# Performance work log

Hardware: AMD Instinct MI355X
Metric: run time of the kernel (lower is better)

## Reference

```python
import jax, jax.numpy as jnp
import numpy as np

B = 4096          # number of sampled constraints (batch)
H = 1024          # hidden_size
N_UNIT = 5
MAXD = 4          # max(DEPTHS)
TAU = 1.0
N_STEPS = N_UNIT * (1 + 2 * MAXD)  # 45
CLIST = np.linspace(10.0, 20.0, 5).astype(np.float32)
NSC = 11
DEPTH_VALS = np.array([2, 3, 4])
RATIO_VALS = np.array([3, 4, 6])
KS_VALS = np.array([3, 5, 7])


def setup_inputs() -> dict:
    key = jax.random.key(0)
    ks = jax.random.split(key, 20)
    def p(k, shape):
        return jax.random.uniform(k, shape, minval=-0.1, maxval=0.1, dtype=jnp.float32)
    return {
        'constraints': jax.random.uniform(ks[0], (B,), minval=10.0, maxval=20.0, dtype=jnp.float32),
        'superclass_id': 3,
        'gumbel_u': jax.random.uniform(ks[1], (N_STEPS, B, 3), minval=1e-6, maxval=1.0 - 1e-6, dtype=jnp.float32),
        'cond_emb': p(ks[2], (len(CLIST), H // 2)),
        'sc_emb': p(ks[3], (NSC, H // 2)),
        'depth_emb': p(ks[4], (3, H)),
        'ratio_emb': p(ks[5], (3, H)),
        'ks_emb': p(ks[6], (3, H)),
        'W_ih': p(ks[7], (4 * H, H)), 'b_ih': p(ks[8], (4 * H,)),
        'W_hh': p(ks[9], (4 * H, H)), 'b_hh': p(ks[10], (4 * H,)),
        'depth_W': p(ks[11], (3, H)), 'depth_b': p(ks[12], (3,)),
        'width_W': p(ks[13], (3, H)), 'width_b': p(ks[14], (3,)),
        'ks_W': p(ks[15], (3, H)), 'ks_b': p(ks[16], (3,)),
    }


def reference(constraints, superclass_id, gumbel_u, cond_emb, sc_emb, depth_emb, ratio_emb,
              ks_emb, W_ih, b_ih, W_hh, b_hh, depth_W, depth_b, width_W, width_b, ks_W, ks_b):
    clist = jnp.asarray(CLIST)
    # linear_interpolation: find bracketing interval for each constraint
    idx = jnp.clip(jnp.searchsorted(clist, constraints, side='right') - 1, 0, clist.shape[0] - 2)
    left, right = clist[idx], clist[idx + 1]
    w = ((right - constraints) / (right - left))[:, None]
    cemb = w * cond_emb[idx] + (1.0 - w) * cond_emb[idx + 1]          # [B, H/2]
    sce = jnp.broadcast_to(sc_emb[superclass_id], (constraints.shape[0], sc_emb.shape[1]))
    embed = jnp.concatenate([cemb, sce], axis=1)                       # [B, H]
    h = jnp.zeros((constraints.shape[0], H), embed.dtype)
    c = h

    def lstm(x, h, c):
        gates = x @ W_ih.T + b_ih + h @ W_hh.T + b_hh                  # [B, 4H]
        i, f, g, o = jnp.split(gates, 4, axis=-1)
        c2 = jax.nn.sigmoid(f) * c + jax.nn.sigmoid(i) * jnp.tanh(g)
        h2 = jax.nn.sigmoid(o) * jnp.tanh(c2)
        return h2, c2

    def gsample(logits, u):
        g = -jnp.log(-jnp.log(u))
        y_soft = jax.nn.softmax((logits + g) / TAU, axis=-1)
        onehot = jax.nn.one_hot(jnp.argmax(y_soft, -1), logits.shape[-1], dtype=y_soft.dtype)
        y_hard = onehot - jax.lax.stop_gradient(y_soft) + y_soft       # straight-through
        return jnp.argmax(y_hard, -1), y_soft, y_hard

    t = 0
    d_idx, d_probs, d_wbs = [], [], []
    r_idx, r_probs, r_wbs = [], [], []
    k_idx, k_probs, k_wbs = [], [], []
    for _unit in range(N_UNIT):
        h, c = lstm(embed, h, c)
        s, ys, yh = gsample(h @ depth_W.T + depth_b, gumbel_u[t]); t += 1
        d_idx.append(s); d_probs.append(ys); d_wbs.append(yh)
        embed = depth_emb[s]
        for _blk in range(MAXD):
            h, c = lstm(embed, h, c)
            s, ys, yh = gsample(h @ width_W.T + width_b, gumbel_u[t]); t += 1
            r_idx.append(s); r_probs.append(ys); r_wbs.append(yh)
            embed = ratio_emb[s]
            h, c = lstm(embed, h, c)
            s, ys, yh = gsample(h @ ks_W.T + ks_b, gumbel_u[t]); t += 1
            k_idx.append(s); k_probs.append(ys); k_wbs.append(yh)
            embed = ks_emb[s]

    depths = jnp.asarray(DEPTH_VALS)[jnp.stack(d_idx)]   # [5, B]
    ratios = jnp.asarray(RATIO_VALS)[jnp.stack(r_idx)]   # [20, B]
    kss = jnp.asarray(KS_VALS)[jnp.stack(k_idx)]         # [20, B]
    return (depths, ratios, kss,
            jnp.stack(d_wbs), jnp.stack(d_probs),
            jnp.stack(r_wbs), jnp.stack(r_probs),
            jnp.stack(k_wbs), jnp.stack(k_probs))
```

## Files before the change

kernel.cpp:

```cpp
#include <hip/hip_runtime.h>
#include <cmath>

namespace {

typedef _Float16 f16;
typedef f16 f16x8 __attribute__((ext_vector_type(8)));
typedef f16 f16x4 __attribute__((ext_vector_type(4)));
typedef float f32x4 __attribute__((ext_vector_type(4)));

constexpr int B  = 4096;
constexpr int H  = 1024;
constexpr int FH = 4 * H;
constexpr int NSTEPS = 45;
constexpr float INVS = 1.0f / 2048.0f;

__device__ __forceinline__ float sigf(float x) { return 1.0f / (1.0f + expf(-x)); }

struct HL { f16 h, l; };
__device__ __forceinline__ HL split16(float a) {
  float ah = (float)(f16)a;
  if (fabsf(a) < 6.1035156e-5f) ah = 0.0f;
  HL r; r.h = (f16)ah; r.l = (f16)((a - ah) * 2048.0f); return r;
}

__device__ __forceinline__ void async16(f16* lds_dst, const f16* gsrc) {
  __builtin_amdgcn_global_load_lds(
      (const __attribute__((address_space(1))) void*)gsrc,
      (__attribute__((address_space(3))) void*)lds_dst, 16, 0, 0);
}

__global__ void convertW_kernel(const float* __restrict__ W,
                                f16* __restrict__ Whi, f16* __restrict__ Wlo) {
  size_t i = ((size_t)blockIdx.x * 256 + threadIdx.x) * 4;
  float4 v = *(const float4*)(W + i);
  HL a = split16(v.x), b = split16(v.y), c = split16(v.z), d = split16(v.w);
  f16x4 hi = {a.h, b.h, c.h, d.h};
  f16x4 lo = {a.l, b.l, c.l, d.l};
  *(f16x4*)(Whi + i) = hi;
  *(f16x4*)(Wlo + i) = lo;
}

__global__ void precompute_kernel(
    const float* __restrict__ W_ih, const float* __restrict__ b_ih, const float* __restrict__ b_hh,
    const float* __restrict__ depth_emb, const float* __restrict__ ratio_emb, const float* __restrict__ ks_emb,
    const float* __restrict__ cond_emb, const float* __restrict__ sc_emb, const int* __restrict__ sid_p,
    float* __restrict__ tblD, float* __restrict__ tblR, float* __restrict__ tblK,
    float* __restrict__ condp, float* __restrict__ base0) {
  const int w4   = threadIdx.x >> 6;
  const int lane = threadIdx.x & 63;
  const int j    = blockIdx.x * 4 + w4;
  const float* wr = W_ih + (size_t)j * H;
  const int k = lane * 16;
  float4 wv0 = *(const float4*)(wr + k);
  float4 wv1 = *(const float4*)(wr + k + 4);
  float4 wv2 = *(const float4*)(wr + k + 8);
  float4 wv3 = *(const float4*)(wr + k + 12);

  auto dot = [&](const float* e) -> float {
    float4 e0 = *(const float4*)(e);
    float4 e1 = *(const float4*)(e + 4);
    float4 e2 = *(const float4*)(e + 8);
    float4 e3 = *(const float4*)(e + 12);
    return e0.x*wv0.x + e0.y*wv0.y + e0.z*wv0.z + e0.w*wv0.w
         + e1.x*wv1.x + e1.y*wv1.y + e1.z*wv1.z + e1.w*wv1.w
         + e2.x*wv2.x + e2.y*wv2.y + e2.z*wv2.z + e2.w*wv2.w
         + e3.x*wv3.x + e3.y*wv3.y + e3.z*wv3.z + e3.w*wv3.w;
  };

  float a[15];
  a[0] = dot(depth_emb + k);       a[1] = dot(depth_emb + H + k);   a[2] = dot(depth_emb + 2*H + k);
  a[3] = dot(ratio_emb + k);       a[4] = dot(ratio_emb + H + k);   a[5] = dot(ratio_emb + 2*H + k);
  a[6] = dot(ks_emb + k);          a[7] = dot(ks_emb + H + k);      a[8] = dot(ks_emb + 2*H + k);
  a[9] = a[10] = a[11] = a[12] = a[13] = a[14] = 0.0f;
  constexpr int HH = H / 2;
  int sid = sid_p[0];
  if (lane < 32) {
    a[9]  = dot(cond_emb + 0*HH + k);
    a[10] = dot(cond_emb + 1*HH + k);
    a[11] = dot(cond_emb + 2*HH + k);
    a[12] = dot(cond_emb + 3*HH + k);
    a[13] = dot(cond_emb + 4*HH + k);
  } else {
    a[14] = dot(sc_emb + sid*HH + (k - HH));
  }
  #pragma unroll
  for (int i = 0; i < 15; ++i) {
    #pragma unroll
    for (int off = 32; off > 0; off >>= 1) a[i] += __shfl_xor(a[i], off);
  }
  if (lane == 0) {
    float bias = b_ih[j] + b_hh[j];
    tblD[0*FH+j]=a[0]+bias; tblD[1*FH+j]=a[1]+bias; tblD[2*FH+j]=a[2]+bias;
    tblR[0*FH+j]=a[3]+bias; tblR[1*FH+j]=a[4]+bias; tblR[2*FH+j]=a[5]+bias;
    tblK[0*FH+j]=a[6]+bias; tblK[1*FH+j]=a[7]+bias; tblK[2*FH+j]=a[8]+bias;
    condp[0*FH+j]=a[9]; condp[1*FH+j]=a[10]; condp[2*FH+j]=a[11];
    condp[3*FH+j]=a[12]; condp[4*FH+j]=a[13];
    base0[j] = a[14] + bias;
  }
}

__global__ void step0_kernel(const float* __restrict__ constraints,
                             const float* __restrict__ condp, const float* __restrict__ base0,
                             f16* __restrict__ hhi, f16* __restrict__ hlo, float* __restrict__ c) {
  int idx = blockIdx.x * blockDim.x + threadIdx.x;
  int b = idx >> 10;
  int j = idx & (H - 1);
  float cv = constraints[b];
  int i0 = 0;
  if (cv >= 12.5f) i0 = 1;
  if (cv >= 15.0f) i0 = 2;
  if (cv >= 17.5f) i0 = 3;
  float right = 10.0f + 2.5f * (float)(i0 + 1);
  float w = (right - cv) / 2.5f;
  const float* c0 = condp + (size_t)i0 * FH;
  const float* c1 = c0 + FH;
  float iw = 1.0f - w;
  float xi = w*c0[j]       + iw*c1[j]       + base0[j];
  float xg = w*c0[2*H+j]   + iw*c1[2*H+j]   + base0[2*H+j];
  float xo = w*c0[3*H+j]   + iw*c1[3*H+j]   + base0[3*H+j];
  float cn = sigf(xi) * tanhf(xg);
  float hn = sigf(xo) * tanhf(cn);
  c[idx] = cn;
  HL s = split16(hn);
  hhi[idx] = s.h; hlo[idx] = s.l;
}

constexpr int BUFE = 24576;

__global__ __launch_bounds__(512, 2) void lstm_step_mfma(
    const f16* __restrict__ hhi, const f16* __restrict__ hlo,
    f16* __restrict__ nhhi, f16* __restrict__ nhlo,
    float* __restrict__ cbuf,
    const f16* __restrict__ Whi, const f16* __restrict__ Wlo,
    const float* __restrict__ tbl, const int* __restrict__ sel) {
  __shared__ __align__(16) f16 lds[3 * BUFE];

  const int tid  = threadIdx.x;
  const int lane = tid & 63;
  const int w    = tid >> 6;
  const int wm   = w >> 1, wn = w & 1;
  const int l15  = lane & 15;
  const int kq   = lane >> 4;

  const int L   = blockIdx.x;
  const int xcd = L & 7, seq = L >> 3;
  const int jb  = (xcd << 2) + (seq & 3);
  const int bb  = seq >> 2;
  const int b0  = bb << 8;
  const int j0  = jb << 5;

  f32x4 accH[4][4] = {};
  f32x4 accL[4][4] = {};

  int offA[4], offB[4];
  #pragma unroll
  for (int mf = 0; mf < 4; ++mf) {
    int R = wm * 64 + mf * 16 + l15;
    int c = kq ^ (R & 3) ^ ((R >> 2) & 3);
    offA[mf] = R * 32 + c * 8;
  }
  #pragma unroll
  for (int nf = 0; nf < 4; ++nf) {
    int R = nf * 32 + wn * 16 + l15;
    int c = kq ^ (R & 3) ^ ((R >> 2) & 3);
    offB[nf] = 16384 + R * 32 + c * 8;
  }

  const int rs = tid >> 2, cs = tid & 3;
  const int r1 = 128 + rs;
  const int cl0 = cs ^ (rs & 3) ^ ((rs >> 2) & 3);
  const int cl1 = cs ^ (r1 & 3) ^ ((r1 >> 2) & 3);
  const int wrow = ((rs >> 5) << 10) + j0 + (rs & 31);
  const f16* sA0h = hhi + (size_t)(b0 + rs) * H + cl0 * 8;
  const f16* sA0l = hlo + (size_t)(b0 + rs) * H + cl0 * 8;
  const f16* sA1h = hhi + (size_t)(b0 + r1) * H + cl1 * 8;
  const f16* sA1l = hlo + (size_t)(b0 + r1) * H + cl1 * 8;
  const f16* sBh  = Whi + (size_t)wrow * H + cl0 * 8;
  const f16* sBl  = Wlo + (size_t)wrow * H + cl0 * 8;
  const int dA0 = w * 512, dA1 = 4096 + w * 512, dB = 16384 + w * 512;

  auto stage6 = [&](f16* buf, int ko) {
    async16(buf + dA0,        sA0h + ko);
    async16(buf + dA0 + 8192, sA0l + ko);
    async16(buf + dA1,        sA1h + ko);
    async16(buf + dA1 + 8192, sA1l + ko);
    async16(buf + dB,         sBh + ko);
    async16(buf + dB + 4096,  sBl + ko);
  };

  f16 *bA = lds, *bB = lds + BUFE, *bC = lds + 2 * BUFE;
  stage6(bA, 0);
  stage6(bB, 32);
  asm volatile("s_waitcnt vmcnt(6)" ::: "memory");
  __builtin_amdgcn_s_barrier();

  for (int kt = 0; kt < 32; ++kt) {
    if (kt < 30) stage6(bC, (kt + 2) * 32);

    f16x8 bh[4], bl[4];
    #pragma unroll
    for (int nf = 0; nf < 4; ++nf) {
      bh[nf] = *(const f16x8*)(bA + offB[nf]);
      bl[nf] = *(const f16x8*)(bA + offB[nf] + 4096);
    }
    #pragma unroll
    for (int mf = 0; mf < 4; ++mf) {
      f16x8 ah = *(const f16x8*)(bA + offA[mf]);
      f16x8 al = *(const f16x8*)(bA + offA[mf] + 8192);
      #pragma unroll
      for (int nf = 0; nf < 4; ++nf) {
        accH[mf][nf] = __builtin_amdgcn_mfma_f32_16x16x32_f16(ah, bh[nf], accH[mf][nf], 0, 0, 0);
        accL[mf][nf] = __builtin_amdgcn_mfma_f32_16x16x32_f16(ah, bl[nf], accL[mf][nf], 0, 0, 0);
        accL[mf][nf] = __builtin_amdgcn_mfma_f32_16x16x32_f16(al, bh[nf], accL[mf][nf], 0, 0, 0);
      }
    }

    if (kt < 30)       asm volatile("s_waitcnt vmcnt(6)" ::: "memory");
    else if (kt == 30) asm volatile("s_waitcnt vmcnt(0)" ::: "memory");
    if (kt < 31) __builtin_amdgcn_s_barrier();

    f16* t = bA; bA = bB; bB = bC; bC = t;
  }

  const int j = j0 + wn * 16 + l15;
  #pragma unroll
  for (int mf = 0; mf < 4; ++mf) {
    #pragma unroll
    for (int r = 0; r < 4; ++r) {
      int b = b0 + wm * 64 + mf * 16 + kq * 4 + r;
      int s = sel[b];
      const float* t = tbl + (size_t)s * FH + j;
      float gi = accH[mf][0][r] + accL[mf][0][r] * INVS + t[0];
      float gf = accH[mf][1][r] + accL[mf][1][r] * INVS + t[H];
      float gg = accH[mf][2][r] + accL[mf][2][r] * INVS + t[2*H];
      float go = accH[mf][3][r] + accL[mf][3][r] * INVS + t[3*H];
      size_t off = (size_t)b * H + j;
      float cp = cbuf[off];
      float cn = sigf(gf) * cp + sigf(gi) * tanhf(gg);
      float hn = sigf(go) * tanhf(cn);
      cbuf[off] = cn;
      HL sp = split16(hn);
      nhhi[off] = sp.h;
      nhlo[off] = sp.l;
    }
  }
}

__global__ void sampler_kernel(const f16* __restrict__ hhi, const f16* __restrict__ hlo,
                               const float* __restrict__ selW, const float* __restrict__ selb,
                               const float* __restrict__ gu,
                               float* __restrict__ val_out, float* __restrict__ wb_out,
                               float* __restrict__ p_out,
                               float v0, float v1, float v2,
                               int* __restrict__ sel) {
  int wave = threadIdx.x >> 6;
  int lane = threadIdx.x & 63;
  int b = blockIdx.x * 4 + wave;
  const f16* hh = hhi + (size_t)b * H;
  const f16* hl = hlo + (size_t)b * H;
  float acc0 = 0, acc1 = 0, acc2 = 0;
  #pragma unroll
  for (int ch = 0; ch < 4; ++ch) {
    int k = ch * 256 + lane * 4;
    f16x4 vh = *(const f16x4*)(hh + k);
    f16x4 vl = *(const f16x4*)(hl + k);
    float x0 = (float)vh[0] + (float)vl[0] * INVS;
    float x1 = (float)vh[1] + (float)vl[1] * INVS;
    float x2 = (float)vh[2] + (float)vl[2] * INVS;
    float x3 = (float)vh[3] + (float)vl[3] * INVS;
    float4 w0 = *(const float4*)(selW + k);
    float4 w1 = *(const float4*)(selW + H + k);
    float4 w2 = *(const float4*)(selW + 2*H + k);
    acc0 += x0*w0.x + x1*w0.y + x2*w0.z + x3*w0.w;
    acc1 += x0*w1.x + x1*w1.y + x2*w1.z + x3*w1.w;
    acc2 += x0*w2.x + x1*w2.y + x2*w2.z + x3*w2.w;
  }
  #pragma unroll
  for (int off = 32; off > 0; off >>= 1) {
    acc0 += __shfl_xor(acc0, off);
    acc1 += __shfl_xor(acc1, off);
    acc2 += __shfl_xor(acc2, off);
  }
  if (lane == 0) {
    float y0 = acc0 + selb[0] - logf(-logf(gu[(size_t)b*3 + 0]));
    float y1 = acc1 + selb[1] - logf(-logf(gu[(size_t)b*3 + 1]));
    float y2 = acc2 + selb[2] - logf(-logf(gu[(size_t)b*3 + 2]));
    int s = 0;
    float best = y0;
    if (y1 > best) { s = 1; best = y1; }
    if (y2 > best) { s = 2; best = y2; }
    float e0 = expf(y0 - best), e1 = expf(y1 - best), e2 = expf(y2 - best);
    float inv = 1.0f / (e0 + e1 + e2);
    float p0 = e0 * inv, p1 = e1 * inv, p2 = e2 * inv;
    val_out[b] = (s == 0) ? v0 : ((s == 1) ? v1 : v2);
    wb_out[(size_t)b*3 + 0] = (s == 0) ? 1.0f : 0.0f;
    wb_out[(size_t)b*3 + 1] = (s == 1) ? 1.0f : 0.0f;
    wb_out[(size_t)b*3 + 2] = (s == 2) ? 1.0f : 0.0f;
    p_out[(size_t)b*3 + 0] = p0;
    p_out[(size_t)b*3 + 1] = p1;
    p_out[(size_t)b*3 + 2] = p2;
    sel[b] = s;
  }
}

}

extern "C" void kernel_launch(void* const* d_in, const int* in_sizes, int n_in,
                              void* d_out, int out_size, void* d_ws, size_t ws_size,
                              hipStream_t stream) {
  (void)in_sizes; (void)n_in; (void)out_size; (void)ws_size;
  const float* constraints = (const float*)d_in[0];
  const int*   sid         = (const int*)d_in[1];
  const float* gumbel      = (const float*)d_in[2];
  const float* cond_emb    = (const float*)d_in[3];
  const float* sc_emb      = (const float*)d_in[4];
  const float* depth_emb   = (const float*)d_in[5];
  const float* ratio_emb   = (const float*)d_in[6];
  const float* ks_emb      = (const float*)d_in[7];
  const float* W_ih        = (const float*)d_in[8];
  const float* b_ih        = (const float*)d_in[9];
  const float* W_hh        = (const float*)d_in[10];
  const float* b_hh        = (const float*)d_in[11];
  const float* depth_W     = (const float*)d_in[12];
  const float* depth_b     = (const float*)d_in[13];
  const float* width_W     = (const float*)d_in[14];
  const float* width_b     = (const float*)d_in[15];
  const float* ks_W        = (const float*)d_in[16];
  const float* ks_b        = (const float*)d_in[17];

  float* out = (float*)d_out;
  float* ws  = (float*)d_ws;

  float* cb    = ws;
  f16*   W16hi = (f16*)(cb + (size_t)B * H);
  f16*   W16lo = W16hi + (size_t)FH * H;
  f16*   hhiA  = W16lo + (size_t)FH * H;
  f16*   hloA  = hhiA + (size_t)B * H;
  f16*   hhiB  = hloA + (size_t)B * H;
  f16*   hloB  = hhiB + (size_t)B * H;
  float* tblD  = (float*)(hloB + (size_t)B * H);
  float* tblR  = tblD + 3 * FH;
  float* tblK  = tblR + 3 * FH;
  float* condp = tblK + 3 * FH;
  float* base0 = condp + 5 * FH;
  int*   sel   = (int*)(base0 + FH);

  convertW_kernel<<<(FH * H / 4) / 256, 256, 0, stream>>>(W_hh, W16hi, W16lo);
  precompute_kernel<<<FH / 4, 256, 0, stream>>>(
      W_ih, b_ih, b_hh, depth_emb, ratio_emb, ks_emb, cond_emb, sc_emb, sid,
      tblD, tblR, tblK, condp, base0);
  step0_kernel<<<(B * H) / 256, 256, 0, stream>>>(constraints, condp, base0, hhiA, hloA, cb);

  const float* selW_arr[3] = {depth_W, width_W, ks_W};
  const float* selb_arr[3] = {depth_b, width_b, ks_b};
  const float vals[3][3]   = {{2.f,3.f,4.f},{3.f,4.f,6.f},{3.f,5.f,7.f}};
  float* tbl_arr[3]        = {tblD, tblR, tblK};

  const size_t DEPTHS = 0,            RATIOS = (size_t)5*B,   KSS    = (size_t)25*B,
               DWBS   = (size_t)45*B, DPROBS = (size_t)60*B,
               RWBS   = (size_t)75*B, RPROBS = (size_t)135*B,
               KWBS   = (size_t)195*B, KPROBS = (size_t)255*B;

  f16* hhi_cur = hhiA; f16* hlo_cur = hloA;
  f16* hhi_nxt = hhiB; f16* hlo_nxt = hloB;
  for (int t = 0; t < NSTEPS; ++t) {
    if (t > 0) {
      int pt = (t - 1) % 9;
      int ptype = (pt == 0) ? 0 : ((pt & 1) ? 1 : 2);
      lstm_step_mfma<<<512, 512, 0, stream>>>(
          hhi_cur, hlo_cur, hhi_nxt, hlo_nxt, cb, W16hi, W16lo, tbl_arr[ptype], sel);
      f16* th = hhi_cur; hhi_cur = hhi_nxt; hhi_nxt = th;
      f16* tl = hlo_cur; hlo_cur = hlo_nxt; hlo_nxt = tl;
    }
    int r = t % 9, u = t / 9;
    int ty, row;
    float *valp, *wbp, *pp;
    if (r == 0)      { ty = 0; row = u;
      valp = out + DEPTHS + (size_t)row*B; wbp = out + DWBS + (size_t)row*B*3; pp = out + DPROBS + (size_t)row*B*3; }
    else if (r & 1)  { ty = 1; row = u*4 + (r-1)/2;
      valp = out + RATIOS + (size_t)row*B; wbp = out + RWBS + (size_t)row*B*3; pp = out + RPROBS + (size_t)row*B*3; }
    else             { ty = 2; row = u*4 + (r-2)/2;
      valp = out + KSS + (size_t)row*B;    wbp = out + KWBS + (size_t)row*B*3; pp = out + KPROBS + (size_t)row*B*3; }
    sampler_kernel<<<B / 4, 256, 0, stream>>>(
        hhi_cur, hlo_cur, selW_arr[ty], selb_arr[ty], gumbel + (size_t)t * B * 3,
        valp, wbp, pp, vals[ty][0], vals[ty][1], vals[ty][2], sel);
  }
}
```

Measured before the change: 5.417 ms.

## Pre-pack W_hh into MFMA fragment layout and load B operands directly to registers

The recurrent weight matrix is now converted once into a fragment-ordered packed layout, so each wave can read its MFMA B operands straight from global memory into registers instead of staging them through LDS. The hi-part fragments are double-buffered in registers one K-tile ahead, while LDS holds only the h activations, which shrinks the shared buffer. The MFMA order is also regrouped by precision part. This removes LDS traffic and bank pressure for the weights but makes each wave wait on global or L2 latency for its weight loads and raises register usage.

```diff
diff --git a/kernel.cpp b/kernel.cpp
--- a/kernel.cpp
+++ b/kernel.cpp
@@ -29,15 +29,25 @@
       (__attribute__((address_space(3))) void*)lds_dst, 16, 0, 0);
 }
 
-__global__ void convertW_kernel(const float* __restrict__ W,
-                                f16* __restrict__ Whi, f16* __restrict__ Wlo) {
-  size_t i = ((size_t)blockIdx.x * 256 + threadIdx.x) * 4;
-  float4 v = *(const float4*)(W + i);
-  HL a = split16(v.x), b = split16(v.y), c = split16(v.z), d = split16(v.w);
-  f16x4 hi = {a.h, b.h, c.h, d.h};
-  f16x4 lo = {a.l, b.l, c.l, d.l};
-  *(f16x4*)(Whi + i) = hi;
-  *(f16x4*)(Wlo + i) = lo;
+__global__ void packW_kernel(const float* __restrict__ W, f16* __restrict__ packed) {
+  int tid  = blockIdx.x * 256 + threadIdx.x;
+  int lane = tid & 63;
+  int rest = tid >> 6;
+  int hl = rest & 1;
+  int nf = (rest >> 1) & 3;
+  int wn = (rest >> 3) & 1;
+  int kt = (rest >> 4) & 31;
+  int jb = rest >> 9;
+  int row = nf * 1024 + jb * 32 + wn * 16 + (lane & 15);
+  int kk  = kt * 32 + (lane >> 4) * 8;
+  const float* src = W + (size_t)row * H + kk;
+  f16x8 v;
+  #pragma unroll
+  for (int i = 0; i < 8; ++i) {
+    HL s = split16(src[i]);
+    v[i] = hl ? s.l : s.h;
+  }
+  *(f16x8*)(packed + (size_t)tid * 8) = v;
 }
 
 __global__ void precompute_kernel(
@@ -125,15 +135,15 @@
   hhi[idx] = s.h; hlo[idx] = s.l;
 }
 
-constexpr int BUFE = 24576;
+constexpr int ABUF = 16384;
 
 __global__ __launch_bounds__(512, 2) void lstm_step_mfma(
     const f16* __restrict__ hhi, const f16* __restrict__ hlo,
     f16* __restrict__ nhhi, f16* __restrict__ nhlo,
     float* __restrict__ cbuf,
-    const f16* __restrict__ Whi, const f16* __restrict__ Wlo,
+    const f16* __restrict__ packW,
     const float* __restrict__ tbl, const int* __restrict__ sel) {
-  __shared__ __align__(16) f16 lds[3 * BUFE];
+  __shared__ __align__(16) f16 lds[3 * ABUF];
 
   const int tid  = threadIdx.x;
   const int lane = tid & 63;
@@ -152,74 +162,79 @@
   f32x4 accH[4][4] = {};
   f32x4 accL[4][4] = {};
 
-  int offA[4], offB[4];
+  int offA[4];
   #pragma unroll
   for (int mf = 0; mf < 4; ++mf) {
     int R = wm * 64 + mf * 16 + l15;
     int c = kq ^ (R & 3) ^ ((R >> 2) & 3);
     offA[mf] = R * 32 + c * 8;
   }
-  #pragma unroll
-  for (int nf = 0; nf < 4; ++nf) {
-    int R = nf * 32 + wn * 16 + l15;
-    int c = kq ^ (R & 3) ^ ((R >> 2) & 3);
-    offB[nf] = 16384 + R * 32 + c * 8;
-  }
 
   const int rs = tid >> 2, cs = tid & 3;
   const int r1 = 128 + rs;
   const int cl0 = cs ^ (rs & 3) ^ ((rs >> 2) & 3);
   const int cl1 = cs ^ (r1 & 3) ^ ((r1 >> 2) & 3);
-  const int wrow = ((rs >> 5) << 10) + j0 + (rs & 31);
   const f16* sA0h = hhi + (size_t)(b0 + rs) * H + cl0 * 8;
   const f16* sA0l = hlo + (size_t)(b0 + rs) * H + cl0 * 8;
   const f16* sA1h = hhi + (size_t)(b0 + r1) * H + cl1 * 8;
   const f16* sA1l = hlo + (size_t)(b0 + r1) * H + cl1 * 8;
-  const f16* sBh  = Whi + (size_t)wrow * H + cl0 * 8;
-  const f16* sBl  = Wlo + (size_t)wrow * H + cl0 * 8;
-  const int dA0 = w * 512, dA1 = 4096 + w * 512, dB = 16384 + w * 512;
-
-  auto stage6 = [&](f16* buf, int ko) {
+  const int dA0 = w * 512, dA1 = 4096 + w * 512;
+
+  auto stageA = [&](f16* buf, int ko) {
     async16(buf + dA0,        sA0h + ko);
     async16(buf + dA0 + 8192, sA0l + ko);
     async16(buf + dA1,        sA1h + ko);
     async16(buf + dA1 + 8192, sA1l + ko);
-    async16(buf + dB,         sBh + ko);
-    async16(buf + dB + 4096,  sBl + ko);
   };
 
-  f16 *bA = lds, *bB = lds + BUFE, *bC = lds + 2 * BUFE;
-  stage6(bA, 0);
-  stage6(bB, 32);
-  asm volatile("s_waitcnt vmcnt(6)" ::: "memory");
+  const f16* wbase = packW + (size_t)jb * 262144 + wn * 4096 + lane * 8;
+
+  f16 *bA = lds, *bB = lds + ABUF, *bC = lds + 2 * ABUF;
+  f16x8 bhA[4], bhB[4];
+
+  stageA(bA, 0);
+  stageA(bB, 32);
+  #pragma unroll
+  for (int nf = 0; nf < 4; ++nf) bhA[nf] = *(const f16x8*)(wbase + nf * 1024);
+  asm volatile("s_waitcnt vmcnt(8)" ::: "memory");
   __builtin_amdgcn_s_barrier();
 
-  for (int kt = 0; kt < 32; ++kt) {
-    if (kt < 30) stage6(bC, (kt + 2) * 32);
-
-    f16x8 bh[4], bl[4];
-    #pragma unroll
-    for (int nf = 0; nf < 4; ++nf) {
-      bh[nf] = *(const f16x8*)(bA + offB[nf]);
-      bl[nf] = *(const f16x8*)(bA + offB[nf] + 4096);
+  auto tile = [&](int kt, f16x8 (&bhC)[4], f16x8 (&bhN)[4]) {
+    if (kt + 2 < 32) stageA(bC, (kt + 2) * 32);
+    const f16* wt = wbase + (size_t)kt * 8192;
+    f16x8 bl[4];
+    #pragma unroll
+    for (int nf = 0; nf < 4; ++nf) bl[nf] = *(const f16x8*)(wt + nf * 1024 + 512);
+    if (kt + 1 < 32) {
+      #pragma unroll
+      for (int nf = 0; nf < 4; ++nf) bhN[nf] = *(const f16x8*)(wt + 8192 + nf * 1024);
     }
+    f16x8 ah[4], al[4];
     #pragma unroll
     for (int mf = 0; mf < 4; ++mf) {
-      f16x8 ah = *(const f16x8*)(bA + offA[mf]);
-      f16x8 al = *(const f16x8*)(bA + offA[mf] + 8192);
+      ah[mf] = *(const f16x8*)(bA + offA[mf]);
+      al[mf] = *(const f16x8*)(bA + offA[mf] + 8192);
+    }
+    #pragma unroll
+    for (int mf = 0; mf < 4; ++mf)
+      #pragma unroll
+      for (int nf = 0; nf < 4; ++nf)
+        accH[mf][nf] = __builtin_amdgcn_mfma_f32_16x16x32_f16(ah[mf], bhC[nf], accH[mf][nf], 0, 0, 0);
+    #pragma unroll
+    for (int mf = 0; mf < 4; ++mf)
       #pragma unroll
       for (int nf = 0; nf < 4; ++nf) {
-        accH[mf][nf] = __builtin_amdgcn_mfma_f32_16x16x32_f16(ah, bh[nf], accH[mf][nf], 0, 0, 0);
-        accL[mf][nf] = __builtin_amdgcn_mfma_f32_16x16x32_f16(ah, bl[nf], accL[mf][nf], 0, 0, 0);
-        accL[mf][nf] = __builtin_amdgcn_mfma_f32_16x16x32_f16(al, bh[nf], accL[mf][nf], 0, 0, 0);
+        accL[mf][nf] = __builtin_amdgcn_mfma_f32_16x16x32_f16(ah[mf], bl[nf], accL[mf][nf], 0, 0, 0);
+        accL[mf][nf] = __builtin_amdgcn_mfma_f32_16x16x32_f16(al[mf], bhC[nf], accL[mf][nf], 0, 0, 0);
       }
-    }
-
-    if (kt < 30)       asm volatile("s_waitcnt vmcnt(6)" ::: "memory");
-    else if (kt == 30) asm volatile("s_waitcnt vmcnt(0)" ::: "memory");
-    if (kt < 31) __builtin_amdgcn_s_barrier();
-
+    asm volatile("s_waitcnt vmcnt(8)" ::: "memory");
+    __builtin_amdgcn_s_barrier();
     f16* t = bA; bA = bB; bB = bC; bC = t;
+  };
+
+  for (int kt = 0; kt < 32; kt += 2) {
+    tile(kt,     bhA, bhB);
+    tile(kt + 1, bhB, bhA);
   }
 
   const int j = j0 + wn * 16 + l15;
@@ -332,9 +347,8 @@
   float* ws  = (float*)d_ws;
 
   float* cb    = ws;
-  f16*   W16hi = (f16*)(cb + (size_t)B * H);
-  f16*   W16lo = W16hi + (size_t)FH * H;
-  f16*   hhiA  = W16lo + (size_t)FH * H;
+  f16*   packW = (f16*)(cb + (size_t)B * H);
+  f16*   hhiA  = packW + (size_t)8 * 1024 * 1024;
   f16*   hloA  = hhiA + (size_t)B * H;
   f16*   hhiB  = hloA + (size_t)B * H;
   f16*   hloB  = hhiB + (size_t)B * H;
@@ -345,7 +359,7 @@
   float* base0 = condp + 5 * FH;
   int*   sel   = (int*)(base0 + FH);
 
-  convertW_kernel<<<(FH * H / 4) / 256, 256, 0, stream>>>(W_hh, W16hi, W16lo);
+  packW_kernel<<<4096, 256, 0, stream>>>(W_hh, packW);
   precompute_kernel<<<FH / 4, 256, 0, stream>>>(
       W_ih, b_ih, b_hh, depth_emb, ratio_emb, ks_emb, cond_emb, sc_emb, sid,
       tblD, tblR, tblK, condp, base0);
@@ -368,7 +382,7 @@
       int pt = (t - 1) % 9;
       int ptype = (pt == 0) ? 0 : ((pt & 1) ? 1 : 2);
       lstm_step_mfma<<<512, 512, 0, stream>>>(
-          hhi_cur, hlo_cur, hhi_nxt, hlo_nxt, cb, W16hi, W16lo, tbl_arr[ptype], sel);
+          hhi_cur, hlo_cur, hhi_nxt, hlo_nxt, cb, packW, tbl_arr[ptype], sel);
       f16* th = hhi_cur; hhi_cur = hhi_nxt; hhi_nxt = th;
       f16* tl = hlo_cur; hlo_cur = hlo_nxt; hlo_nxt = tl;
     }
```

Result: slower. 5.659 ms (+4.5%).
